# Optimization experiments

Hardware: AMD Instinct MI355X
Metric: run time of the kernel (lower is better)

Reference implementation:

```python
import jax, jax.numpy as jnp
import numpy as np
import math

B, S, D, H = 2, 2048, 1024, 16
HD = D // H  # head_dim = 64
NEG = -1.0e9


def _xavier(key, shape, gain):
    fan_in, fan_out = shape[1], shape[0]
    bound = gain * math.sqrt(6.0 / (fan_in + fan_out))
    return jax.random.uniform(key, shape, jnp.float32, -bound, bound)


def setup_inputs() -> dict:
    key = jax.random.key(0)
    ks = jax.random.split(key, 7)
    gain = 1.0 / math.sqrt(2.0)
    q = jax.random.normal(ks[0], (B, S, D), jnp.float32)
    pad_mask = jax.random.randint(ks[1], (B, S), 0, 2) > 0  # True = masked key
    # ensure not all keys masked per row
    pad_mask = pad_mask.at[:, 0].set(False)
    Wq = _xavier(ks[2], (D, D), gain)
    Wk = _xavier(ks[3], (D, D), gain)
    Wv = _xavier(ks[4], (D, D), gain)
    Wo = _xavier(ks[5], (D, D), gain)
    bk = jax.random.normal(ks[6], (4, D), jnp.float32) * 0.02
    return {"q": q, "pad_mask": pad_mask,
            "Wq": Wq, "bq": bk[0], "Wk": Wk, "bk": bk[1],
            "Wv": Wv, "bv": bk[2], "Wo": Wo, "bo": bk[3]}


def reference(q, pad_mask, Wq, bq, Wk, bk, Wv, bv, Wo, bo):
    # Self-attention: k = v = q (k, v args are None in this config)
    x = q
    # torch Linear: y = x @ W.T + b
    qh = (x @ Wq.T + bq).reshape(B, S, H, HD).transpose(0, 2, 1, 3)  # [B,H,S,HD]
    kh = (x @ Wk.T + bk).reshape(B, S, H, HD).transpose(0, 2, 1, 3)
    vh = (x @ Wv.T + bv).reshape(B, S, H, HD).transpose(0, 2, 1, 3)

    scores = jnp.einsum('bhqd,bhkd->bhqk', qh, kh) / math.sqrt(HD)  # [B,H,S,S]
    causal = jnp.triu(jnp.ones((S, S), bool), k=1)                  # [S,S]
    scores = jnp.where(causal[None, None], NEG, scores)
    scores = jnp.where(pad_mask[:, None, None, :], NEG, scores)

    probs = jax.nn.softmax(scores, axis=-1)
    out = jnp.einsum('bhqk,bhkd->bhqd', probs, vh)                  # [B,H,S,HD]
    out = out.transpose(0, 2, 1, 3).reshape(B, S, D)
    return out @ Wo.T + bo
```

## Files before the change

kernel.cpp:

```cpp
#include <hip/hip_runtime.h>
#include <hip/hip_bf16.h>

#define BB 2
#define SS 2048
#define DD 1024
#define HH 16
#define HD 64
#define MM (BB * SS)
#define NQKV 3072

typedef __attribute__((ext_vector_type(8))) short short8;
typedef __attribute__((ext_vector_type(4))) short s16x4;
typedef __attribute__((ext_vector_type(4))) float floatx4;
typedef __attribute__((ext_vector_type(4))) float f32x4;
using bf16 = __hip_bfloat16;

__device__ __forceinline__ float b2f(bf16 x) { return __bfloat162float(x); }
__device__ __forceinline__ short f2bs(float x) {
    bf16 h = __float2bfloat16(x);
    return *reinterpret_cast<short*>(&h);
}
__device__ __forceinline__ float bs2f(short s) {
    bf16 h; *reinterpret_cast<short*>(&h) = s; return __bfloat162float(h);
}

__device__ __forceinline__ int lds_off(int row, int chunk) {
    return row * 64 + ((chunk ^ (row & 7)) * 8);
}

#define GL16(gp, lp)                                                        \
    __builtin_amdgcn_global_load_lds(                                       \
        (const __attribute__((address_space(1))) void*)(gp),                \
        (__attribute__((address_space(3))) void*)(lp), 16, 0, 0)

#define N_WCAT (NQKV * DD / 4)
#define N_X    (MM * DD / 4)
#define N_WOB  (DD * DD / 4)

__global__ __launch_bounds__(256) void convert_all(
    const float* __restrict__ Wq, const float* __restrict__ Wk,
    const float* __restrict__ Wv, const float* __restrict__ X,
    const float* __restrict__ Wo,
    short* __restrict__ wcat, short* __restrict__ xb, short* wob)
{
    const int total = N_WCAT + N_X + (wob ? N_WOB : 0);
    const int stride = gridDim.x * blockDim.x;
    for (int i = blockIdx.x * blockDim.x + threadIdx.x; i < total; i += stride) {
        f32x4 v; short* dp;
        if (i < N_WCAT) {
            const int e = i * 4;
            const int z = e >> 20;
            const int off = e & 0xFFFFF;
            const float* src = (z == 0) ? Wq : (z == 1) ? Wk : Wv;
            v = *(const f32x4*)(src + off);
            dp = wcat + e;
        } else if (i < N_WCAT + N_X) {
            const int e = (i - N_WCAT) * 4;
            v = *(const f32x4*)(X + e);
            dp = xb + e;
        } else {
            const int e = (i - N_WCAT - N_X) * 4;
            v = *(const f32x4*)(Wo + e);
            dp = wob + e;
        }
        s16x4 o; o[0] = f2bs(v[0]); o[1] = f2bs(v[1]); o[2] = f2bs(v[2]); o[3] = f2bs(v[3]);
        *(s16x4*)dp = o;
    }
}

__global__ __launch_bounds__(256) void convert_w(
    const float* __restrict__ W, short* __restrict__ dst)
{
    const int stride = gridDim.x * blockDim.x;
    for (int i = blockIdx.x * blockDim.x + threadIdx.x; i < DD * DD / 4; i += stride) {
        f32x4 v = *(const f32x4*)(W + i * 4);
        s16x4 o; o[0] = f2bs(v[0]); o[1] = f2bs(v[1]); o[2] = f2bs(v[2]); o[3] = f2bs(v[3]);
        *(s16x4*)(dst + i * 4) = o;
    }
}

__global__ __launch_bounds__(256) void build_idx(
    const int* __restrict__ pad, int* __restrict__ cidx, int* __restrict__ pfx)
{
    const int b   = blockIdx.x;
    const int tid = threadIdx.x;
    __shared__ int part[256];
    const int* pr = pad + b * SS;
    int* ci = cidx + b * SS;
    int* pf = pfx + b * SS;

    const int s0 = tid * 8;
    int loc[8]; int sum = 0;
#pragma unroll
    for (int j = 0; j < 8; ++j) { loc[j] = (pr[s0 + j] == 0) ? 1 : 0; sum += loc[j]; }
    part[tid] = sum;
    __syncthreads();
    for (int off = 1; off < 256; off <<= 1) {
        const int v   = part[tid];
        const int add = (tid >= off) ? part[tid - off] : 0;
        __syncthreads();
        part[tid] = v + add;
        __syncthreads();
    }
    int run = (tid > 0) ? part[tid - 1] : 0;
#pragma unroll
    for (int j = 0; j < 8; ++j) {
        run += loc[j];
        pf[s0 + j] = run;
        if (loc[j]) ci[run - 1] = s0 + j;
    }
    const int total = part[255];
    for (int j = total + tid; j < SS; j += 256) ci[j] = SS;
}

__global__ __launch_bounds__(256, 6) void qkv_gemm2(
    const short* __restrict__ Xb, const short* __restrict__ Wcat,
    const float* __restrict__ bq, const float* __restrict__ bk, const float* __restrict__ bv,
    const int* __restrict__ pad, const int* __restrict__ pfx,
    bf16* __restrict__ outQ, bf16* __restrict__ outKc, bf16* __restrict__ outVTc)
{
    __shared__ short As[128 * 64];
    __shared__ short Bs[64 * 64];

    const int tid  = threadIdx.x;
    const int lane = tid & 63;
    const int wave = tid >> 6;
    const int wm   = wave & 1;
    const int wn   = wave >> 1;
    const int g    = lane >> 4;
    const int fr   = lane & 15;

    const int m0 = blockIdx.x * 128;
    const int n0 = blockIdx.y * 64;

    const int l8  = lane >> 3;
    const int sch = (lane & 7) ^ l8;
    const short* agl = Xb   + (size_t)(m0 + l8) * DD + sch * 8;
    const short* bgl = Wcat + (size_t)(n0 + l8) * DD + sch * 8;

    floatx4 acc[4][2];
#pragma unroll
    for (int i = 0; i < 4; ++i)
#pragma unroll
        for (int j = 0; j < 2; ++j) acc[i][j] = (floatx4){0.f, 0.f, 0.f, 0.f};

    for (int kb = 0; kb < DD; kb += 64) {
        __syncthreads();
#pragma unroll
        for (int j = 0; j < 4; ++j) {
            const int r = wave * 32 + j * 8;
            GL16(agl + (size_t)r * DD + kb, &As[r * 64]);
        }
#pragma unroll
        for (int j = 0; j < 2; ++j) {
            const int r = wave * 16 + j * 8;
            GL16(bgl + (size_t)r * DD + kb, &Bs[r * 64]);
        }
        __syncthreads();

#pragma unroll
        for (int kk = 0; kk < 2; ++kk) {
            const int kc = kk * 4 + g;
            short8 af[4], bf[2];
#pragma unroll
            for (int t = 0; t < 4; ++t)
                af[t] = *(const short8*)&As[lds_off(wm * 64 + t * 16 + fr, kc)];
#pragma unroll
            for (int u = 0; u < 2; ++u)
                bf[u] = *(const short8*)&Bs[lds_off(wn * 32 + u * 16 + fr, kc)];
#pragma unroll
            for (int mt = 0; mt < 4; ++mt)
#pragma unroll
                for (int nt = 0; nt < 2; ++nt)
                    acc[mt][nt] = __builtin_amdgcn_mfma_f32_16x16x32_bf16(
                        af[mt], bf[nt], acc[mt][nt], 0, 0, 0);
        }
    }

#pragma unroll
    for (int nt = 0; nt < 2; ++nt) {
        const int n  = n0 + wn * 32 + nt * 16 + fr;
        const int z  = n >> 10;
        const int nn = n & 1023;
        const int h_ = nn >> 6;
        const int d_ = nn & 63;
        const float biasv = ((z == 0) ? bq : (z == 1) ? bk : bv)[nn];
#pragma unroll
        for (int mt = 0; mt < 4; ++mt) {
#pragma unroll
            for (int reg = 0; reg < 4; ++reg) {
                const int m  = m0 + wm * 64 + mt * 16 + g * 4 + reg;
                const int b_ = m >> 11;
                const int s_ = m & (SS - 1);
                const float v = acc[mt][nt][reg] + biasv;
                if (z == 0) {
                    outQ[((size_t)((b_ * HH + h_) * SS + s_)) * HD + d_] =
                        __float2bfloat16(v);
                } else if (pad[b_ * SS + s_] == 0) {
                    const int cs = pfx[b_ * SS + s_] - 1;
                    if (z == 1)
                        outKc[((size_t)((b_ * HH + h_) * SS + cs)) * HD + d_] =
                            __float2bfloat16(v);
                    else
                        outVTc[((size_t)((b_ * HH + h_) * HD + d_)) * SS + cs] =
                            __float2bfloat16(v);
                }
            }
        }
    }
}

__global__ __launch_bounds__(256, 6) void o_gemm2(
    const short* __restrict__ A, const short* __restrict__ Wob,
    const float* __restrict__ bias, float* __restrict__ out)
{
    __shared__ short As[128 * 64];
    __shared__ short Bs[64 * 64];

    const int tid  = threadIdx.x;
    const int lane = tid & 63;
    const int wave = tid >> 6;
    const int wm   = wave & 1;
    const int wn   = wave >> 1;
    const int g    = lane >> 4;
    const int fr   = lane & 15;

    const int m0 = blockIdx.x * 128;
    const int n0 = blockIdx.y * 64;

    const int l8  = lane >> 3;
    const int sch = (lane & 7) ^ l8;
    const short* agl = A   + (size_t)(m0 + l8) * DD + sch * 8;
    const short* bgl = Wob + (size_t)(n0 + l8) * DD + sch * 8;

    floatx4 acc[4][2];
#pragma unroll
    for (int i = 0; i < 4; ++i)
#pragma unroll
        for (int j = 0; j < 2; ++j) acc[i][j] = (floatx4){0.f, 0.f, 0.f, 0.f};

    for (int kb = 0; kb < DD; kb += 64) {
        __syncthreads();
#pragma unroll
        for (int j = 0; j < 4; ++j) {
            const int r = wave * 32 + j * 8;
            GL16(agl + (size_t)r * DD + kb, &As[r * 64]);
        }
#pragma unroll
        for (int j = 0; j < 2; ++j) {
            const int r = wave * 16 + j * 8;
            GL16(bgl + (size_t)r * DD + kb, &Bs[r * 64]);
        }
        __syncthreads();

#pragma unroll
        for (int kk = 0; kk < 2; ++kk) {
            const int kc = kk * 4 + g;
            short8 af[4], bf[2];
#pragma unroll
            for (int t = 0; t < 4; ++t)
                af[t] = *(const short8*)&As[lds_off(wm * 64 + t * 16 + fr, kc)];
#pragma unroll
            for (int u = 0; u < 2; ++u)
                bf[u] = *(const short8*)&Bs[lds_off(wn * 32 + u * 16 + fr, kc)];
#pragma unroll
            for (int mt = 0; mt < 4; ++mt)
#pragma unroll
                for (int nt = 0; nt < 2; ++nt)
                    acc[mt][nt] = __builtin_amdgcn_mfma_f32_16x16x32_bf16(
                        af[mt], bf[nt], acc[mt][nt], 0, 0, 0);
        }
    }

#pragma unroll
    for (int nt = 0; nt < 2; ++nt) {
        const int n = n0 + wn * 32 + nt * 16 + fr;
        const float biasv = bias[n];
#pragma unroll
        for (int mt = 0; mt < 4; ++mt) {
#pragma unroll
            for (int reg = 0; reg < 4; ++reg) {
                const int m = m0 + wm * 64 + mt * 16 + g * 4 + reg;
                out[(size_t)m * DD + n] = acc[mt][nt][reg] + biasv;
            }
        }
    }
}

__global__ __launch_bounds__(256) void flash_mfma9(
    const bf16* __restrict__ Qh,
    const bf16* __restrict__ Kc,
    const bf16* __restrict__ VTc,
    const int*  __restrict__ cidx,
    const int*  __restrict__ pfx,
    bf16* __restrict__ attn)
{
    __shared__ short Ks[2][64 * 64];
    __shared__ short Vs[2][64 * 64];
    __shared__ short Pld[4][16 * 64];

    const int tid  = threadIdx.x;
    const int lane = tid & 63;
    const int wave = tid >> 6;
    const int xcd = blockIdx.x & 7;
    const int idx = blockIdx.x >> 3;
    const int bh  = (xcd << 2) | (idx & 3);
    const int qt  = 31 - (idx >> 2);
    const int q0  = qt * 64 + wave * 16;
    const int b_  = bh >> 4;
    const int h_  = bh & 15;

    const int g  = lane >> 4;
    const int fr = lane & 15;
    const int k8 = g * 8;

    short* myP = Pld[wave];

    const bf16* qbase = Qh + ((size_t)bh * SS + q0 + fr) * HD + k8;
    short8 qf[2];
#pragma unroll
    for (int hh = 0; hh < 2; ++hh) {
        short8 rawq = *(const short8*)((const short*)qbase + hh * 32);
#pragma unroll
        for (int j = 0; j < 8; ++j) qf[hh][j] = f2bs(bs2f(rawq[j]) * 0.125f);
    }

    const int* corow = cidx + b_ * SS;
    const int nkeys  = pfx[b_ * SS + qt * 64 + 63];
    const short* kbh = (const short*)(Kc  + (size_t)bh * SS * HD);
    const short* vbh = (const short*)(VTc + (size_t)bh * HD * SS);

    const int l8  = lane >> 3;
    const int sch = (lane & 7) ^ l8;
    auto stageKV = [&](int buf, int kb) {
#pragma unroll
        for (int j = 0; j < 2; ++j) {
            const int r = wave * 16 + j * 8;
            GL16(kbh + (size_t)(kb + r + l8) * HD + sch * 8, &Ks[buf][r * 64]);
            GL16(vbh + (size_t)(r + l8) * SS + kb + sch * 8, &Vs[buf][r * 64]);
        }
    };

    floatx4 o[4] = {{0,0,0,0},{0,0,0,0},{0,0,0,0},{0,0,0,0}};
    float l_acc[4] = {0.f, 0.f, 0.f, 0.f};

    stageKV(0, 0);
    asm volatile("s_waitcnt vmcnt(0)" ::: "memory");
    __syncthreads();

    for (int kb = 0; kb < nkeys; kb += 64) {
        const int cur = (kb >> 6) & 1;
        if (kb + 64 < nkeys) stageKV(cur ^ 1, kb + 64);

        const short* Kt = Ks[cur];
        const short* Vc = Vs[cur];

        floatx4 c[4];
        __builtin_amdgcn_s_setprio(1);
#pragma unroll
        for (int t = 0; t < 4; ++t) {
            short8 kf0 = *(const short8*)&Kt[(t * 16 + fr) * 64 + ((g       ^ (fr & 7)) << 3)];
            short8 kf1 = *(const short8*)&Kt[(t * 16 + fr) * 64 + (((g + 4) ^ (fr & 7)) << 3)];
            floatx4 cc = {0, 0, 0, 0};
            cc = __builtin_amdgcn_mfma_f32_16x16x32_bf16(qf[0], kf0, cc, 0, 0, 0);
            cc = __builtin_amdgcn_mfma_f32_16x16x32_bf16(qf[1], kf1, cc, 0, 0, 0);
            c[t] = cc;
        }
        __builtin_amdgcn_s_setprio(0);

        int ko[4];
#pragma unroll
        for (int t = 0; t < 4; ++t) ko[t] = corow[kb + t * 16 + fr];

#pragma unroll
        for (int reg = 0; reg < 4; ++reg) {
            const int q   = q0 + g * 4 + reg;
            const int row = g * 4 + reg;
#pragma unroll
            for (int t = 0; t < 4; ++t) {
                const float p = (ko[t] <= q) ? __expf(c[t][reg]) : 0.f;
                l_acc[reg] += p;
                const int col = t * 16 + fr;
                myP[row * 64 + (((col >> 3) ^ (row & 7)) << 3) + (col & 7)] = f2bs(p);
            }
        }

        short8 pf0 = *(const short8*)&myP[fr * 64 + ((g       ^ (fr & 7)) << 3)];
        short8 pf1 = *(const short8*)&myP[fr * 64 + (((g + 4) ^ (fr & 7)) << 3)];
        __builtin_amdgcn_s_setprio(1);
#pragma unroll
        for (int n = 0; n < 4; ++n) {
            short8 vf0 = *(const short8*)&Vc[(n * 16 + fr) * 64 + ((g       ^ (fr & 7)) << 3)];
            short8 vf1 = *(const short8*)&Vc[(n * 16 + fr) * 64 + (((g + 4) ^ (fr & 7)) << 3)];
            o[n] = __builtin_amdgcn_mfma_f32_16x16x32_bf16(pf0, vf0, o[n], 0, 0, 0);
            o[n] = __builtin_amdgcn_mfma_f32_16x16x32_bf16(pf1, vf1, o[n], 0, 0, 0);
        }
        __builtin_amdgcn_s_setprio(0);

        asm volatile("s_waitcnt vmcnt(0)" ::: "memory");
        __syncthreads();
    }

    float inv[4];
#pragma unroll
    for (int reg = 0; reg < 4; ++reg) {
        float l = l_acc[reg];
#pragma unroll
        for (int off = 1; off < 16; off <<= 1) l += __shfl_xor(l, off);
        inv[reg] = 1.f / fmaxf(l, 1e-38f);
    }
#pragma unroll
    for (int n = 0; n < 4; ++n) {
#pragma unroll
        for (int reg = 0; reg < 4; ++reg) {
            const int q = q0 + g * 4 + reg;
            attn[((size_t)(b_ * SS + q)) * DD + h_ * HD + n * 16 + fr] =
                __float2bfloat16(o[n][reg] * inv[reg]);
        }
    }
}

extern "C" void kernel_launch(void* const* d_in, const int* in_sizes, int n_in,
                              void* d_out, int out_size, void* d_ws, size_t ws_size,
                              hipStream_t stream) {
    const float* x   = (const float*)d_in[0];
    const int*   pad = (const int*)  d_in[1];
    const float* Wq  = (const float*)d_in[2];
    const float* bq  = (const float*)d_in[3];
    const float* Wk  = (const float*)d_in[4];
    const float* bk  = (const float*)d_in[5];
    const float* Wv  = (const float*)d_in[6];
    const float* bv  = (const float*)d_in[7];
    const float* Wo  = (const float*)d_in[8];
    const float* bo  = (const float*)d_in[9];
    float* out = (float*)d_out;

    const size_t NELEM = (size_t)BB * HH * SS * HD;
    bf16* Qh   = (bf16*)d_ws;
    bf16* Kc   = Qh + NELEM;
    bf16* VTc  = Kc + NELEM;
    bf16* attn = VTc + NELEM;
    int*  cidx = (int*)(attn + NELEM);
    int*  pfx  = cidx + BB * SS;
    short* Wcat = (short*)d_out;
    short* Xb   = (short*)d_out + (size_t)NQKV * DD;

    const size_t ws_need = 4 * NELEM * sizeof(bf16) + 2 * (size_t)BB * SS * sizeof(int)
                         + (size_t)DD * DD * sizeof(short);
    const bool big_ws = ws_size >= ws_need;
    short* Wob = big_ws ? (short*)(pfx + BB * SS) : (short*)Qh;

    convert_all<<<2048, 256, 0, stream>>>(Wq, Wk, Wv, x, Wo, Wcat, Xb,
                                          big_ws ? Wob : nullptr);

    build_idx<<<BB, 256, 0, stream>>>(pad, cidx, pfx);

    hipMemsetAsync(Kc, 0, 2 * NELEM * sizeof(bf16), stream);

    dim3 gq(MM / 128, NQKV / 64);
    qkv_gemm2<<<gq, 256, 0, stream>>>(Xb, Wcat, bq, bk, bv, pad, pfx,
                                      Qh, Kc, VTc);

    flash_mfma9<<<BB * HH * 32, 256, 0, stream>>>(Qh, Kc, VTc, cidx, pfx, attn);

    if (!big_ws) convert_w<<<512, 256, 0, stream>>>(Wo, Wob);

    dim3 go(MM / 128, DD / 64);
    o_gemm2<<<go, 256, 0, stream>>>((const short*)attn, Wob, bo, out);
}
```

Before: 189.4 us.

## Fold pad-index scan into convert kernel and drop K/V memset via tail zero writes

```diff
diff --git a/kernel.cpp b/kernel.cpp
--- a/kernel.cpp
+++ b/kernel.cpp
@@ -40,12 +40,46 @@
 __global__ __launch_bounds__(256) void convert_all(
     const float* __restrict__ Wq, const float* __restrict__ Wk,
     const float* __restrict__ Wv, const float* __restrict__ X,
-    const float* __restrict__ Wo,
+    const float* __restrict__ Wo, const int* __restrict__ pad,
+    int* __restrict__ cidx, int* __restrict__ pfx,
     short* __restrict__ wcat, short* __restrict__ xb, short* wob)
 {
+    if (blockIdx.x < BB) {
+        const int b   = blockIdx.x;
+        const int tid = threadIdx.x;
+        __shared__ int part[256];
+        const int* pr = pad + b * SS;
+        int* ci = cidx + b * SS;
+        int* pf = pfx + b * SS;
+
+        const int s0 = tid * 8;
+        int loc[8]; int sum = 0;
+#pragma unroll
+        for (int j = 0; j < 8; ++j) { loc[j] = (pr[s0 + j] == 0) ? 1 : 0; sum += loc[j]; }
+        part[tid] = sum;
+        __syncthreads();
+        for (int off = 1; off < 256; off <<= 1) {
+            const int v   = part[tid];
+            const int add = (tid >= off) ? part[tid - off] : 0;
+            __syncthreads();
+            part[tid] = v + add;
+            __syncthreads();
+        }
+        int run = (tid > 0) ? part[tid - 1] : 0;
+#pragma unroll
+        for (int j = 0; j < 8; ++j) {
+            run += loc[j];
+            pf[s0 + j] = run;
+            if (loc[j]) ci[run - 1] = s0 + j;
+        }
+        const int total = part[255];
+        for (int j = total + tid; j < SS; j += 256) ci[j] = SS;
+        return;
+    }
+
     const int total = N_WCAT + N_X + (wob ? N_WOB : 0);
-    const int stride = gridDim.x * blockDim.x;
-    for (int i = blockIdx.x * blockDim.x + threadIdx.x; i < total; i += stride) {
+    const int stride = (gridDim.x - BB) * blockDim.x;
+    for (int i = (blockIdx.x - BB) * blockDim.x + threadIdx.x; i < total; i += stride) {
         f32x4 v; short* dp;
         if (i < N_WCAT) {
             const int e = i * 4;
@@ -79,40 +113,6 @@
     }
 }
 
-__global__ __launch_bounds__(256) void build_idx(
-    const int* __restrict__ pad, int* __restrict__ cidx, int* __restrict__ pfx)
-{
-    const int b   = blockIdx.x;
-    const int tid = threadIdx.x;
-    __shared__ int part[256];
-    const int* pr = pad + b * SS;
-    int* ci = cidx + b * SS;
-    int* pf = pfx + b * SS;
-
-    const int s0 = tid * 8;
-    int loc[8]; int sum = 0;
-#pragma unroll
-    for (int j = 0; j < 8; ++j) { loc[j] = (pr[s0 + j] == 0) ? 1 : 0; sum += loc[j]; }
-    part[tid] = sum;
-    __syncthreads();
-    for (int off = 1; off < 256; off <<= 1) {
-        const int v   = part[tid];
-        const int add = (tid >= off) ? part[tid - off] : 0;
-        __syncthreads();
-        part[tid] = v + add;
-        __syncthreads();
-    }
-    int run = (tid > 0) ? part[tid - 1] : 0;
-#pragma unroll
-    for (int j = 0; j < 8; ++j) {
-        run += loc[j];
-        pf[s0 + j] = run;
-        if (loc[j]) ci[run - 1] = s0 + j;
-    }
-    const int total = part[255];
-    for (int j = total + tid; j < SS; j += 256) ci[j] = SS;
-}
-
 __global__ __launch_bounds__(256, 6) void qkv_gemm2(
     const short* __restrict__ Xb, const short* __restrict__ Wcat,
     const float* __restrict__ bq, const float* __restrict__ bk, const float* __restrict__ bv,
@@ -177,6 +177,9 @@
         }
     }
 
+    const int bblk = m0 >> 11;
+    const int btot = pfx[bblk * SS + SS - 1];
+
 #pragma unroll
     for (int nt = 0; nt < 2; ++nt) {
         const int n  = n0 + wn * 32 + nt * 16 + fr;
@@ -190,20 +193,20 @@
 #pragma unroll
             for (int reg = 0; reg < 4; ++reg) {
                 const int m  = m0 + wm * 64 + mt * 16 + g * 4 + reg;
-                const int b_ = m >> 11;
                 const int s_ = m & (SS - 1);
                 const float v = acc[mt][nt][reg] + biasv;
                 if (z == 0) {
-                    outQ[((size_t)((b_ * HH + h_) * SS + s_)) * HD + d_] =
+                    outQ[((size_t)((bblk * HH + h_) * SS + s_)) * HD + d_] =
                         __float2bfloat16(v);
-                } else if (pad[b_ * SS + s_] == 0) {
-                    const int cs = pfx[b_ * SS + s_] - 1;
+                } else {
+                    const int ps  = pfx[bblk * SS + s_];
+                    const bool um = (pad[bblk * SS + s_] == 0);
+                    const int cs  = um ? (ps - 1) : (btot + s_ - ps);
+                    const short w = um ? f2bs(v) : (short)0;
                     if (z == 1)
-                        outKc[((size_t)((b_ * HH + h_) * SS + cs)) * HD + d_] =
-                            __float2bfloat16(v);
+                        ((short*)outKc)[((size_t)((bblk * HH + h_) * SS + cs)) * HD + d_] = w;
                     else
-                        outVTc[((size_t)((b_ * HH + h_) * HD + d_)) * SS + cs] =
-                            __float2bfloat16(v);
+                        ((short*)outVTc)[((size_t)((bblk * HH + h_) * HD + d_)) * SS + cs] = w;
                 }
             }
         }
@@ -450,12 +453,9 @@
     const bool big_ws = ws_size >= ws_need;
     short* Wob = big_ws ? (short*)(pfx + BB * SS) : (short*)Qh;
 
-    convert_all<<<2048, 256, 0, stream>>>(Wq, Wk, Wv, x, Wo, Wcat, Xb,
-                                          big_ws ? Wob : nullptr);
-
-    build_idx<<<BB, 256, 0, stream>>>(pad, cidx, pfx);
-
-    hipMemsetAsync(Kc, 0, 2 * NELEM * sizeof(bf16), stream);
+    convert_all<<<2048 + BB, 256, 0, stream>>>(Wq, Wk, Wv, x, Wo, pad,
+                                               cidx, pfx, Wcat, Xb,
+                                               big_ws ? Wob : nullptr);
 
     dim3 gq(MM / 128, NQKV / 64);
     qkv_gemm2<<<gq, 256, 0, stream>>>(Xb, Wcat, bq, bk, bv, pad, pfx,
```

Measured after the change: 184.1 us. -2.8%, faster.
